# Kernel optimization log

Hardware: AMD Instinct MI355X
Metric: run time of the kernel (lower is better)

The kernel has to match this reference:

```python
import jax, jax.numpy as jnp
import numpy as np

B, S, D = 4, 4096, 2048
NUM_MODALITIES = 2


def setup_inputs() -> dict:
    key = jax.random.key(0)
    k_x, k_t, k_w0, k_b0, k_w1, k_b1 = jax.random.split(key, 6)
    scale = 1.0 / np.sqrt(D)
    return {
        "hidden_states": jax.random.normal(k_x, (B, S, D), dtype=jnp.float32),
        "type_ids": jax.random.randint(k_t, (B, S), 0, NUM_MODALITIES, dtype=jnp.int32),
        "W0": jax.random.uniform(k_w0, (D, D), jnp.float32, -scale, scale),
        "b0": jax.random.uniform(k_b0, (D,), jnp.float32, -scale, scale),
        "W1": jax.random.uniform(k_w1, (D, D), jnp.float32, -scale, scale),
        "b1": jax.random.uniform(k_b1, (D,), jnp.float32, -scale, scale),
    }


def reference(hidden_states, type_ids, W0, b0, W1, b1):
    # Original: gather tokens where type_ids == i, apply expert i's Linear,
    # scatter into a zero-init [B, S, out_dim] buffer. The masks partition
    # all tokens, so this equals a masked mixture of the two dense GEMMs.
    y0 = jnp.einsum("bsd,ed->bse", hidden_states, W0) + b0  # expert 0
    y1 = jnp.einsum("bsd,ed->bse", hidden_states, W1) + b1  # expert 1
    m0 = (type_ids == 0)[..., None]
    m1 = (type_ids == 1)[..., None]
    zero = jnp.zeros((), dtype=y0.dtype)
    return jnp.where(m0, y0, zero) + jnp.where(m1, y1, zero)
```

## Files before the change

kernel.cpp:

```cpp
#include <hip/hip_runtime.h>
#include <hip/hip_bf16.h>
#include <stdint.h>


#define T_TOK 16384
#define DDIM  2048
#define NT_K  32
#define NT_D  64
#define MT    64
#define NTILE 8

typedef __attribute__((ext_vector_type(4))) float          f32x4;
typedef __attribute__((ext_vector_type(8))) short          bf16x8;
typedef __attribute__((ext_vector_type(2))) unsigned int   u32x2;

#define WS_HBF   0ull
#define WS_W0BF  67108864ull
#define WS_W1BF  75497472ull
#define WS_META  83886080ull
#define WS_IDX   83886208ull
#define WS_NEED  (WS_IDX + 65536ull)

__device__ __forceinline__ unsigned short cvt1_bf16(float f) {
  unsigned u = __builtin_bit_cast(unsigned, f);
  unsigned rnd = 0x7fffu + ((u >> 16) & 1u);
  return (unsigned short)((u + rnd) >> 16);
}

__device__ __forceinline__ void gload_lds16(const void* g, void* l) {
  __builtin_amdgcn_global_load_lds(
      (const __attribute__((address_space(1))) unsigned int*)g,
      (__attribute__((address_space(3))) unsigned int*)l, 16, 0, 0);
}

#define BAR()     asm volatile("s_barrier" ::: "memory")
#define VMCNT2()  asm volatile("s_waitcnt vmcnt(2)" ::: "memory")
#define VMCNT4()  asm volatile("s_waitcnt vmcnt(4)" ::: "memory")
#define VMCNT6()  asm volatile("s_waitcnt vmcnt(6)" ::: "memory")
#define VMCNT0()  asm volatile("s_waitcnt vmcnt(0)" ::: "memory")
#define LGKM0()   asm volatile("s_waitcnt lgkmcnt(0)" ::: "memory")
#define SCHEDBAR() __builtin_amdgcn_sched_barrier(0)

__global__ void k_prep(const float* __restrict__ H, const float* __restrict__ W0,
                       const float* __restrict__ W1, const int* __restrict__ typ,
                       unsigned short* __restrict__ Hbf,
                       unsigned short* __restrict__ W0bf,
                       unsigned short* __restrict__ W1bf,
                       int* __restrict__ meta) {
  const int gid = blockIdx.x * blockDim.x + threadIdx.x;
  if (gid < T_TOK && typ[gid] == 0) atomicAdd(&meta[0], 1);
  const int nH = T_TOK * DDIM / 4;
  const int nW = DDIM * DDIM / 4;
  const int total = nH + 2 * nW;
  const int stride = gridDim.x * blockDim.x;
  for (int i = gid; i < total; i += stride) {
    const float* s; unsigned short* d; int j;
    if (i < nH)           { s = H;  d = Hbf;  j = i; }
    else if (i < nH + nW) { s = W0; d = W0bf; j = i - nH; }
    else                  { s = W1; d = W1bf; j = i - nH - nW; }
    f32x4 v = ((const f32x4*)s)[j];
    unsigned p0 = (unsigned)cvt1_bf16(v[0]) | ((unsigned)cvt1_bf16(v[1]) << 16);
    unsigned p1 = (unsigned)cvt1_bf16(v[2]) | ((unsigned)cvt1_bf16(v[3]) << 16);
    u32x2 o; o[0] = p0; o[1] = p1;
    ((u32x2*)d)[j] = o;
  }
}

__global__ void k_scatter(const int* __restrict__ typ, int* __restrict__ meta,
                          int* __restrict__ idx) {
  int i = blockIdx.x * blockDim.x + threadIdx.x;
  if (i >= T_TOK) return;
  int c0 = meta[0];
  int t = typ[i];
  int pos = (t == 0) ? atomicAdd(&meta[2], 1) : c0 + atomicAdd(&meta[3], 1);
  idx[pos] = i;
}

__global__ __launch_bounds__(512) void k_gemm256(
    const unsigned short* __restrict__ Hbf,
    const unsigned short* __restrict__ W0bf,
    const unsigned short* __restrict__ W1bf,
    const float* __restrict__ B0, const float* __restrict__ B1,
    const int* __restrict__ meta, const int* __restrict__ idx,
    float* __restrict__ OUT)
{
  __shared__ char lds[131072];

  const int orig = blockIdx.x;
  const int wg = (orig & 7) * 64 + (orig >> 3);
  int my = wg >> 3;
  const int bx = wg & 7;

  const int c0 = meta[0];
  int ms = c0 >> 8; if (ms > MT - 1) ms = MT - 1;
  my = (my == 0) ? ms : (my == ms) ? 0 : my;

  const int tid  = threadIdx.x;
  const int lane = tid & 63;
  const int wid  = tid >> 6;
  const int wr   = wid >> 2;
  const int wc   = wid & 3;
  const int fr   = lane & 15;
  const int g    = lane >> 4;

  const int start = my * 256;
  const int isDual = (start < c0 && c0 < start + 256) ? 1 : 0;
  const int e0    = (start >= c0) ? 1 : 0;
  const int colBase = bx * 256;

  const int cs = (lane & 3) ^ ((lane >> 3) & 3);
  const char* aS[2];
  int rt[2];
#pragma unroll
  for (int l = 0; l < 2; ++l) {
    int ch = 2 * wid + l;
    rt[l] = ch * 16 + (lane >> 2);
    int orow = idx[start + rt[l]];
    aS[l] = (const char*)Hbf + (size_t)orow * 4096 + cs * 16;
  }
  const int chB = (2 * wid) * 1024;

  const int sw = (g ^ ((fr >> 1) & 3)) << 4;
  int aF[8], bF[4];
#pragma unroll
  for (int m = 0; m < 8; ++m) aF[m] = ((wr * 128 + m * 16 + fr) << 6) + sw;
#pragma unroll
  for (int n = 0; n < 4; ++n) bF[n] = ((wc * 64 + n * 16 + fr) << 6) + sw;

  f32x4 acc[8][4];
#pragma unroll
  for (int m = 0; m < 8; ++m)
#pragma unroll
    for (int n = 0; n < 4; ++n) acc[m][n] = (f32x4)0.0f;

  int cols[4];
#pragma unroll
  for (int n = 0; n < 4; ++n) cols[n] = colBase + wc * 64 + n * 16 + fr;

  if (!isDual) {
    const unsigned short* Wb = e0 ? W1bf : W0bf;
    const char* wS[2];
#pragma unroll
    for (int l = 0; l < 2; ++l)
      wS[l] = (const char*)(Wb + (size_t)(colBase + rt[l]) * DDIM) + cs * 16;

    auto STAGE_A = [&](int d, int kh, int tn) {
      char* dst = lds + (d << 15) + (kh << 14) + chB;
      int ko = tn * 128 + kh * 64;
      gload_lds16(aS[0] + ko, dst);
      gload_lds16(aS[1] + ko, dst + 1024);
    };
    auto STAGE_B = [&](int d, int kh, int tn) {
      char* dst = lds + 65536 + (d << 15) + (kh << 14) + chB;
      int ko = tn * 128 + kh * 64;
      gload_lds16(wS[0] + ko, dst);
      gload_lds16(wS[1] + ko, dst + 1024);
    };

    STAGE_A(0, 0, 0); STAGE_B(0, 0, 0); STAGE_A(0, 1, 0); STAGE_B(0, 1, 0);
    VMCNT4();
    BAR();

#pragma unroll 2
    for (int t = 0; t < NT_K; ++t) {
      const int c = t & 1, d = c ^ 1;
      int t1 = t + 1; if (t1 == NT_K) t1 = NT_K - 1;
      const char* Ak0 = lds + (c << 15);
      const char* Ak1 = Ak0 + 16384;
      const char* Bk0 = lds + 65536 + (c << 15);
      const char* Bk1 = Bk0 + 16384;

      bf16x8 a[8], bb0, bb1;

#pragma unroll
      for (int m = 0; m < 8; ++m) a[m] = *(const bf16x8*)(Ak0 + aF[m]);
      bb0 = *(const bf16x8*)(Bk0 + bF[0]);
      bb1 = *(const bf16x8*)(Bk0 + bF[1]);
      STAGE_A(d, 0, t1);
      BAR(); LGKM0(); SCHEDBAR();
      __builtin_amdgcn_s_setprio(1);
#pragma unroll
      for (int m = 0; m < 8; ++m) {
        acc[m][0] = __builtin_amdgcn_mfma_f32_16x16x32_bf16(a[m], bb0, acc[m][0], 0, 0, 0);
        acc[m][1] = __builtin_amdgcn_mfma_f32_16x16x32_bf16(a[m], bb1, acc[m][1], 0, 0, 0);
      }
      __builtin_amdgcn_s_setprio(0);

      bb0 = *(const bf16x8*)(Bk0 + bF[2]);
      bb1 = *(const bf16x8*)(Bk0 + bF[3]);
      VMCNT2();
      STAGE_B(d, 0, t1);
      BAR(); LGKM0(); SCHEDBAR();
      __builtin_amdgcn_s_setprio(1);
#pragma unroll
      for (int m = 0; m < 8; ++m) {
        acc[m][2] = __builtin_amdgcn_mfma_f32_16x16x32_bf16(a[m], bb0, acc[m][2], 0, 0, 0);
        acc[m][3] = __builtin_amdgcn_mfma_f32_16x16x32_bf16(a[m], bb1, acc[m][3], 0, 0, 0);
      }
      __builtin_amdgcn_s_setprio(0);

#pragma unroll
      for (int m = 0; m < 8; ++m) a[m] = *(const bf16x8*)(Ak1 + aF[m]);
      bb0 = *(const bf16x8*)(Bk1 + bF[0]);
      bb1 = *(const bf16x8*)(Bk1 + bF[1]);
      STAGE_A(d, 1, t1);
      BAR(); LGKM0(); SCHEDBAR();
      __builtin_amdgcn_s_setprio(1);
#pragma unroll
      for (int m = 0; m < 8; ++m) {
        acc[m][0] = __builtin_amdgcn_mfma_f32_16x16x32_bf16(a[m], bb0, acc[m][0], 0, 0, 0);
        acc[m][1] = __builtin_amdgcn_mfma_f32_16x16x32_bf16(a[m], bb1, acc[m][1], 0, 0, 0);
      }
      __builtin_amdgcn_s_setprio(0);

      bb0 = *(const bf16x8*)(Bk1 + bF[2]);
      bb1 = *(const bf16x8*)(Bk1 + bF[3]);
      VMCNT2();
      STAGE_B(d, 1, t1);
      BAR(); LGKM0(); SCHEDBAR();
      __builtin_amdgcn_s_setprio(1);
#pragma unroll
      for (int m = 0; m < 8; ++m) {
        acc[m][2] = __builtin_amdgcn_mfma_f32_16x16x32_bf16(a[m], bb0, acc[m][2], 0, 0, 0);
        acc[m][3] = __builtin_amdgcn_mfma_f32_16x16x32_bf16(a[m], bb1, acc[m][3], 0, 0, 0);
      }
      __builtin_amdgcn_s_setprio(0);
    }

    VMCNT0();

    const float* Bv = e0 ? B1 : B0;
    float bias[4];
#pragma unroll
    for (int n = 0; n < 4; ++n) bias[n] = Bv[cols[n]];
#pragma unroll
    for (int m = 0; m < 8; ++m) {
      int lb = wr * 128 + m * 16 + (g << 2);
#pragma unroll
      for (int j = 0; j < 4; ++j) {
        int orow = idx[start + lb + j];
        float* op = OUT + (size_t)orow * DDIM;
#pragma unroll
        for (int n = 0; n < 4; ++n) op[cols[n]] = acc[m][n][j] + bias[n];
      }
    }
  } else {
    const char* wS0[2]; const char* wS1[2];
#pragma unroll
    for (int l = 0; l < 2; ++l) {
      wS0[l] = (const char*)(W0bf + (size_t)(colBase + rt[l]) * DDIM) + cs * 16;
      wS1[l] = (const char*)(W1bf + (size_t)(colBase + rt[l]) * DDIM) + cs * 16;
    }
    const int lo_w = c0 - start - wr * 128;
    int mmix = 8;
    if (lo_w > 0 && lo_w < 128 && (lo_w & 15)) mmix = lo_w >> 4;

    f32x4 accX[4];
#pragma unroll
    for (int n = 0; n < 4; ++n) accX[n] = (f32x4)0.0f;

    auto DSTAGE = [&](int d, int tn) {
      int ko = tn * 64;
      char* ad  = lds + (d << 14) + chB;
      char* b0d = lds + 32768 + (d << 14) + chB;
      char* b1d = lds + 65536 + (d << 14) + chB;
      gload_lds16(aS[0] + ko, ad);
      gload_lds16(aS[1] + ko, ad + 1024);
      gload_lds16(wS0[0] + ko, b0d);
      gload_lds16(wS0[1] + ko, b0d + 1024);
      gload_lds16(wS1[0] + ko, b1d);
      gload_lds16(wS1[1] + ko, b1d + 1024);
    };

    DSTAGE(0, 0);
    for (int t = 0; t < NT_D; ++t) {
      const int c = t & 1, d = c ^ 1;
      int t1 = t + 1; if (t1 == NT_D) t1 = NT_D - 1;
      DSTAGE(d, t1);
      VMCNT6();
      BAR();
      const char* Ac  = lds + (c << 14);
      const char* B0c = lds + 32768 + (c << 14);
      const char* B1c = lds + 65536 + (c << 14);
      bf16x8 a[8], b0f[4], b1f[4];
#pragma unroll
      for (int m = 0; m < 8; ++m) a[m] = *(const bf16x8*)(Ac + aF[m]);
#pragma unroll
      for (int n = 0; n < 4; ++n) {
        b0f[n] = *(const bf16x8*)(B0c + bF[n]);
        b1f[n] = *(const bf16x8*)(B1c + bF[n]);
      }
      LGKM0(); SCHEDBAR();
      __builtin_amdgcn_s_setprio(1);
#pragma unroll
      for (int m = 0; m < 8; ++m) {
        if (m == mmix) {
#pragma unroll
          for (int n = 0; n < 4; ++n) {
            acc[m][n] = __builtin_amdgcn_mfma_f32_16x16x32_bf16(a[m], b0f[n], acc[m][n], 0, 0, 0);
            accX[n]   = __builtin_amdgcn_mfma_f32_16x16x32_bf16(a[m], b1f[n], accX[n],   0, 0, 0);
          }
        } else if (m * 16 >= lo_w) {
#pragma unroll
          for (int n = 0; n < 4; ++n)
            acc[m][n] = __builtin_amdgcn_mfma_f32_16x16x32_bf16(a[m], b1f[n], acc[m][n], 0, 0, 0);
        } else {
#pragma unroll
          for (int n = 0; n < 4; ++n)
            acc[m][n] = __builtin_amdgcn_mfma_f32_16x16x32_bf16(a[m], b0f[n], acc[m][n], 0, 0, 0);
        }
      }
      __builtin_amdgcn_s_setprio(0);
      BAR();
    }
    VMCNT0();

    float bias0v[4], bias1v[4];
#pragma unroll
    for (int n = 0; n < 4; ++n) { bias0v[n] = B0[cols[n]]; bias1v[n] = B1[cols[n]]; }
#pragma unroll
    for (int m = 0; m < 8; ++m) {
      int lb = wr * 128 + m * 16 + (g << 2);
      if (m == mmix) {
#pragma unroll
        for (int j = 0; j < 4; ++j) {
          int p = start + lb + j;
          int orow = idx[p];
          float* op = OUT + (size_t)orow * DDIM;
          if (p >= c0) {
#pragma unroll
            for (int n = 0; n < 4; ++n) op[cols[n]] = accX[n][j] + bias1v[n];
          } else {
#pragma unroll
            for (int n = 0; n < 4; ++n) op[cols[n]] = acc[m][n][j] + bias0v[n];
          }
        }
      } else {
        int em = (m * 16 >= lo_w) ? 1 : 0;
#pragma unroll
        for (int j = 0; j < 4; ++j) {
          int orow = idx[start + lb + j];
          float* op = OUT + (size_t)orow * DDIM;
#pragma unroll
          for (int n = 0; n < 4; ++n)
            op[cols[n]] = acc[m][n][j] + (em ? bias1v[n] : bias0v[n]);
        }
      }
    }
  }
}

#define BMd 64
#define BNd 64
#define BKd 32
#define LDW 36

__device__ __forceinline__ bf16x8 cvt_bf16x8(f32x4 lo, f32x4 hi) {
  bf16x8 r;
#pragma unroll
  for (int i = 0; i < 4; ++i) {
    r[i]     = (short)cvt1_bf16(lo[i]);
    r[i + 4] = (short)cvt1_bf16(hi[i]);
  }
  return r;
}

__global__ __launch_bounds__(256, 2) void mot_mfma_diag(
    const float* __restrict__ H,  const int* __restrict__ TYP,
    const float* __restrict__ W0, const float* __restrict__ B0,
    const float* __restrict__ W1, const float* __restrict__ B1,
    float* __restrict__ OUT)
{
  __shared__ float As[BMd * LDW];
  __shared__ float W0s[BNd * LDW];
  __shared__ float W1s[BNd * LDW];

  const int tid = threadIdx.x;
  const int rowBase = blockIdx.y * BMd;
  const int colBase = blockIdx.x * BNd;
  const int srow  = tid >> 3;
  const int scol4 = (tid & 7) << 2;
  const float* hA  = H  + (size_t)(rowBase + srow) * DDIM + scol4;
  const float* hW0 = W0 + (size_t)(colBase + srow) * DDIM + scol4;
  const float* hW1 = W1 + (size_t)(colBase + srow) * DDIM + scol4;

  const int lane = tid & 63;
  const int w    = tid >> 6;
  const int fr   = lane & 15;
  const int g    = lane >> 4;

  f32x4 acc0[4], acc1[4];
#pragma unroll
  for (int m = 0; m < 4; ++m) { acc0[m] = (f32x4)0.0f; acc1[m] = (f32x4)0.0f; }

  for (int k0 = 0; k0 < DDIM; k0 += BKd) {
    f32x4 va[2], v0[2], v1[2];
#pragma unroll
    for (int p = 0; p < 2; ++p) {
      va[p] = *(const f32x4*)(hA  + (size_t)p * 32 * DDIM);
      v0[p] = *(const f32x4*)(hW0 + (size_t)p * 32 * DDIM);
      v1[p] = *(const f32x4*)(hW1 + (size_t)p * 32 * DDIM);
    }
    hA += BKd; hW0 += BKd; hW1 += BKd;
    __syncthreads();
#pragma unroll
    for (int p = 0; p < 2; ++p) {
      int r = srow + 32 * p;
      *(f32x4*)(&As [r * LDW + scol4]) = va[p];
      *(f32x4*)(&W0s[r * LDW + scol4]) = v0[p];
      *(f32x4*)(&W1s[r * LDW + scol4]) = v1[p];
    }
    __syncthreads();

    bf16x8 af[4];
#pragma unroll
    for (int m = 0; m < 4; ++m) {
      const float* ap = &As[(m * 16 + fr) * LDW + g * 8];
      af[m] = cvt_bf16x8(*(const f32x4*)ap, *(const f32x4*)(ap + 4));
    }
    const float* b0p = &W0s[(w * 16 + fr) * LDW + g * 8];
    const float* b1p = &W1s[(w * 16 + fr) * LDW + g * 8];
    bf16x8 bf0 = cvt_bf16x8(*(const f32x4*)b0p, *(const f32x4*)(b0p + 4));
    bf16x8 bf1 = cvt_bf16x8(*(const f32x4*)b1p, *(const f32x4*)(b1p + 4));
#pragma unroll
    for (int m = 0; m < 4; ++m) {
      acc0[m] = __builtin_amdgcn_mfma_f32_16x16x32_bf16(af[m], bf0, acc0[m], 0, 0, 0);
      acc1[m] = __builtin_amdgcn_mfma_f32_16x16x32_bf16(af[m], bf1, acc1[m], 0, 0, 0);
    }
  }

  const int col = colBase + w * 16 + fr;
  const float bz0 = B0[col];
  const float bz1 = B1[col];
#pragma unroll
  for (int m = 0; m < 4; ++m)
#pragma unroll
    for (int j = 0; j < 4; ++j) {
      int row = rowBase + m * 16 + (g << 2) + j;
      int t = TYP[row];
      OUT[(size_t)row * DDIM + col] = (t == 0) ? (acc0[m][j] + bz0) : (acc1[m][j] + bz1);
    }
}

extern "C" void kernel_launch(void* const* d_in, const int* in_sizes, int n_in,
                              void* d_out, int out_size, void* d_ws, size_t ws_size,
                              hipStream_t stream) {
  const float* H   = (const float*)d_in[0];
  const int*   TYP = (const int*)  d_in[1];
  const float* W0  = (const float*)d_in[2];
  const float* B0v = (const float*)d_in[3];
  const float* W1  = (const float*)d_in[4];
  const float* B1v = (const float*)d_in[5];
  float* OUT = (float*)d_out;

  if (ws_size < WS_NEED) {
    dim3 grid(DDIM / BNd, T_TOK / BMd);
    mot_mfma_diag<<<grid, dim3(256), 0, stream>>>(H, TYP, W0, B0v, W1, B1v, OUT);
    return;
  }

  unsigned short* Hbf  = (unsigned short*)((char*)d_ws + WS_HBF);
  unsigned short* W0bf = (unsigned short*)((char*)d_ws + WS_W0BF);
  unsigned short* W1bf = (unsigned short*)((char*)d_ws + WS_W1BF);
  int* meta = (int*)((char*)d_ws + WS_META);
  int* idx  = (int*)((char*)d_ws + WS_IDX);

  hipMemsetAsync(meta, 0, 16, stream);
  k_prep   <<<4096, 256, 0, stream>>>(H, W0, W1, TYP, Hbf, W0bf, W1bf, meta);
  k_scatter<<<64,   256, 0, stream>>>(TYP, meta, idx);
  k_gemm256<<<MT * NTILE, 512, 0, stream>>>(Hbf, W0bf, W1bf, B0v, B1v, meta, idx, OUT);
}
```

Measured before the change: 218.5 us.

## Fuse fp32-to-bf16 conversion of activations into GEMM A-tile staging

Removes the separate pass that converts hidden states to bf16 in a workspace. The GEMM now loads fp32 rows into registers, packs them with v_cvt_pk_bf16_f32, and writes them to LDS, prefetching two k-steps ahead. This drops a full read and write of the 128 MB activation tensor plus the re-read of the bf16 copy, and the prep kernel now converts only the weights. In exchange the GEMM reads twice as many A bytes, converts every A tile once per column block (8 times in total), and the pipeline's waitcnt and barrier placement is reworked, which could expose load latency.

New measurement: 221.2 us. About the same (+1.2%).

```diff
diff --git a/kernel.cpp b/kernel.cpp
--- a/kernel.cpp
+++ b/kernel.cpp
@@ -13,12 +13,12 @@
 typedef __attribute__((ext_vector_type(4))) float          f32x4;
 typedef __attribute__((ext_vector_type(8))) short          bf16x8;
 typedef __attribute__((ext_vector_type(2))) unsigned int   u32x2;
-
-#define WS_HBF   0ull
-#define WS_W0BF  67108864ull
-#define WS_W1BF  75497472ull
-#define WS_META  83886080ull
-#define WS_IDX   83886208ull
+typedef __attribute__((ext_vector_type(4))) unsigned int   u32x4;
+
+#define WS_W0BF  0ull
+#define WS_W1BF  8388608ull
+#define WS_META  16777216ull
+#define WS_IDX   16777344ull
 #define WS_NEED  (WS_IDX + 65536ull)
 
 __device__ __forceinline__ unsigned short cvt1_bf16(float f) {
@@ -27,6 +27,12 @@
   return (unsigned short)((u + rnd) >> 16);
 }
 
+__device__ __forceinline__ unsigned pk2(float lo, float hi) {
+  unsigned r;
+  asm("v_cvt_pk_bf16_f32 %0, %1, %2" : "=v"(r) : "v"(lo), "v"(hi));
+  return r;
+}
+
 __device__ __forceinline__ void gload_lds16(const void* g, void* l) {
   __builtin_amdgcn_global_load_lds(
       (const __attribute__((address_space(1))) unsigned int*)g,
@@ -34,30 +40,25 @@
 }
 
 #define BAR()     asm volatile("s_barrier" ::: "memory")
-#define VMCNT2()  asm volatile("s_waitcnt vmcnt(2)" ::: "memory")
 #define VMCNT4()  asm volatile("s_waitcnt vmcnt(4)" ::: "memory")
-#define VMCNT6()  asm volatile("s_waitcnt vmcnt(6)" ::: "memory")
+#define VMCNT8()  asm volatile("s_waitcnt vmcnt(8)" ::: "memory")
 #define VMCNT0()  asm volatile("s_waitcnt vmcnt(0)" ::: "memory")
 #define LGKM0()   asm volatile("s_waitcnt lgkmcnt(0)" ::: "memory")
 #define SCHEDBAR() __builtin_amdgcn_sched_barrier(0)
 
-__global__ void k_prep(const float* __restrict__ H, const float* __restrict__ W0,
-                       const float* __restrict__ W1, const int* __restrict__ typ,
-                       unsigned short* __restrict__ Hbf,
-                       unsigned short* __restrict__ W0bf,
-                       unsigned short* __restrict__ W1bf,
-                       int* __restrict__ meta) {
+__global__ void k_wprep(const float* __restrict__ W0, const float* __restrict__ W1,
+                        const int* __restrict__ typ,
+                        unsigned short* __restrict__ W0bf,
+                        unsigned short* __restrict__ W1bf,
+                        int* __restrict__ meta) {
   const int gid = blockIdx.x * blockDim.x + threadIdx.x;
   if (gid < T_TOK && typ[gid] == 0) atomicAdd(&meta[0], 1);
-  const int nH = T_TOK * DDIM / 4;
   const int nW = DDIM * DDIM / 4;
-  const int total = nH + 2 * nW;
   const int stride = gridDim.x * blockDim.x;
-  for (int i = gid; i < total; i += stride) {
-    const float* s; unsigned short* d; int j;
-    if (i < nH)           { s = H;  d = Hbf;  j = i; }
-    else if (i < nH + nW) { s = W0; d = W0bf; j = i - nH; }
-    else                  { s = W1; d = W1bf; j = i - nH - nW; }
+  for (int i = gid; i < 2 * nW; i += stride) {
+    const float* s = (i < nW) ? W0 : W1;
+    unsigned short* d = (i < nW) ? W0bf : W1bf;
+    int j = (i < nW) ? i : i - nW;
     f32x4 v = ((const f32x4*)s)[j];
     unsigned p0 = (unsigned)cvt1_bf16(v[0]) | ((unsigned)cvt1_bf16(v[1]) << 16);
     unsigned p1 = (unsigned)cvt1_bf16(v[2]) | ((unsigned)cvt1_bf16(v[3]) << 16);
@@ -77,7 +78,7 @@
 }
 
 __global__ __launch_bounds__(512) void k_gemm256(
-    const unsigned short* __restrict__ Hbf,
+    const float* __restrict__ H,
     const unsigned short* __restrict__ W0bf,
     const unsigned short* __restrict__ W1bf,
     const float* __restrict__ B0, const float* __restrict__ B1,
@@ -109,14 +110,14 @@
   const int colBase = bx * 256;
 
   const int cs = (lane & 3) ^ ((lane >> 3) & 3);
-  const char* aS[2];
+  const char* aS32[2];
   int rt[2];
 #pragma unroll
   for (int l = 0; l < 2; ++l) {
     int ch = 2 * wid + l;
     rt[l] = ch * 16 + (lane >> 2);
     int orow = idx[start + rt[l]];
-    aS[l] = (const char*)Hbf + (size_t)orow * 4096 + cs * 16;
+    aS32[l] = (const char*)H + (size_t)orow * 8192 + cs * 32;
   }
   const int chB = (2 * wid) * 1024;
 
@@ -144,11 +145,30 @@
     for (int l = 0; l < 2; ++l)
       wS[l] = (const char*)(Wb + (size_t)(colBase + rt[l]) * DDIM) + cs * 16;
 
-    auto STAGE_A = [&](int d, int kh, int tn) {
-      char* dst = lds + (d << 15) + (kh << 14) + chB;
-      int ko = tn * 128 + kh * 64;
-      gload_lds16(aS[0] + ko, dst);
-      gload_lds16(aS[1] + ko, dst + 1024);
+    f32x4 av[2][2][2];
+
+    auto ALOAD = [&](int tn) {
+#pragma unroll
+      for (int l = 0; l < 2; ++l)
+#pragma unroll
+        for (int kh = 0; kh < 2; ++kh) {
+          const char* p = aS32[l] + tn * 256 + kh * 128;
+          av[l][kh][0] = *(const f32x4*)p;
+          av[l][kh][1] = *(const f32x4*)(p + 16);
+        }
+    };
+    auto AWRITE = [&](int d) {
+#pragma unroll
+      for (int l = 0; l < 2; ++l)
+#pragma unroll
+        for (int kh = 0; kh < 2; ++kh) {
+          u32x4 w;
+          w[0] = pk2(av[l][kh][0][0], av[l][kh][0][1]);
+          w[1] = pk2(av[l][kh][0][2], av[l][kh][0][3]);
+          w[2] = pk2(av[l][kh][1][0], av[l][kh][1][1]);
+          w[3] = pk2(av[l][kh][1][2], av[l][kh][1][3]);
+          *(u32x4*)(lds + (d << 15) + (kh << 14) + (2 * wid + l) * 1024 + lane * 16) = w;
+        }
     };
     auto STAGE_B = [&](int d, int kh, int tn) {
       char* dst = lds + 65536 + (d << 15) + (kh << 14) + chB;
@@ -157,14 +177,20 @@
       gload_lds16(wS[1] + ko, dst + 1024);
     };
 
-    STAGE_A(0, 0, 0); STAGE_B(0, 0, 0); STAGE_A(0, 1, 0); STAGE_B(0, 1, 0);
-    VMCNT4();
+    ALOAD(0);
+    VMCNT0();
+    AWRITE(0);
+    STAGE_B(0, 0, 0); STAGE_B(0, 1, 0);
+    ALOAD(1);
+    VMCNT8();
+    LGKM0();
     BAR();
 
 #pragma unroll 2
     for (int t = 0; t < NT_K; ++t) {
       const int c = t & 1, d = c ^ 1;
       int t1 = t + 1; if (t1 == NT_K) t1 = NT_K - 1;
+      int t2 = t + 2; if (t2 >= NT_K) t2 = NT_K - 1;
       const char* Ak0 = lds + (c << 15);
       const char* Ak1 = Ak0 + 16384;
       const char* Bk0 = lds + 65536 + (c << 15);
@@ -176,7 +202,7 @@
       for (int m = 0; m < 8; ++m) a[m] = *(const bf16x8*)(Ak0 + aF[m]);
       bb0 = *(const bf16x8*)(Bk0 + bF[0]);
       bb1 = *(const bf16x8*)(Bk0 + bF[1]);
-      STAGE_A(d, 0, t1);
+      STAGE_B(d, 0, t1);
       BAR(); LGKM0(); SCHEDBAR();
       __builtin_amdgcn_s_setprio(1);
 #pragma unroll
@@ -188,8 +214,7 @@
 
       bb0 = *(const bf16x8*)(Bk0 + bF[2]);
       bb1 = *(const bf16x8*)(Bk0 + bF[3]);
-      VMCNT2();
-      STAGE_B(d, 0, t1);
+      STAGE_B(d, 1, t1);
       BAR(); LGKM0(); SCHEDBAR();
       __builtin_amdgcn_s_setprio(1);
 #pragma unroll
@@ -203,8 +228,10 @@
       for (int m = 0; m < 8; ++m) a[m] = *(const bf16x8*)(Ak1 + aF[m]);
       bb0 = *(const bf16x8*)(Bk1 + bF[0]);
       bb1 = *(const bf16x8*)(Bk1 + bF[1]);
-      STAGE_A(d, 1, t1);
-      BAR(); LGKM0(); SCHEDBAR();
+      VMCNT4();
+      AWRITE(d);
+      LGKM0(); SCHEDBAR();
+      BAR();
       __builtin_amdgcn_s_setprio(1);
 #pragma unroll
       for (int m = 0; m < 8; ++m) {
@@ -215,8 +242,8 @@
 
       bb0 = *(const bf16x8*)(Bk1 + bF[2]);
       bb1 = *(const bf16x8*)(Bk1 + bF[3]);
-      VMCNT2();
-      STAGE_B(d, 1, t1);
+      ALOAD(t2);
+      VMCNT8();
       BAR(); LGKM0(); SCHEDBAR();
       __builtin_amdgcn_s_setprio(1);
 #pragma unroll
@@ -259,26 +286,48 @@
 #pragma unroll
     for (int n = 0; n < 4; ++n) accX[n] = (f32x4)0.0f;
 
-    auto DSTAGE = [&](int d, int tn) {
-      int ko = tn * 64;
-      char* ad  = lds + (d << 14) + chB;
+    f32x4 avd[2][2];
+    auto ALOADD = [&](int tn) {
+#pragma unroll
+      for (int l = 0; l < 2; ++l) {
+        const char* p = aS32[l] + tn * 128;
+        avd[l][0] = *(const f32x4*)p;
+        avd[l][1] = *(const f32x4*)(p + 16);
+      }
+    };
+    auto AWRITED = [&](int d) {
+#pragma unroll
+      for (int l = 0; l < 2; ++l) {
+        u32x4 w;
+        w[0] = pk2(avd[l][0][0], avd[l][0][1]);
+        w[1] = pk2(avd[l][0][2], avd[l][0][3]);
+        w[2] = pk2(avd[l][1][0], avd[l][1][1]);
+        w[3] = pk2(avd[l][1][2], avd[l][1][3]);
+        *(u32x4*)(lds + (d << 14) + (2 * wid + l) * 1024 + lane * 16) = w;
+      }
+    };
+    auto STAGE_BD = [&](int d, int tn) {
       char* b0d = lds + 32768 + (d << 14) + chB;
       char* b1d = lds + 65536 + (d << 14) + chB;
-      gload_lds16(aS[0] + ko, ad);
-      gload_lds16(aS[1] + ko, ad + 1024);
-      gload_lds16(wS0[0] + ko, b0d);
-      gload_lds16(wS0[1] + ko, b0d + 1024);
-      gload_lds16(wS1[0] + ko, b1d);
-      gload_lds16(wS1[1] + ko, b1d + 1024);
+      gload_lds16(wS0[0] + tn * 64, b0d);
+      gload_lds16(wS0[1] + tn * 64, b0d + 1024);
+      gload_lds16(wS1[0] + tn * 64, b1d);
+      gload_lds16(wS1[1] + tn * 64, b1d + 1024);
     };
 
-    DSTAGE(0, 0);
+    ALOADD(0);
+    VMCNT0();
+    AWRITED(0);
+    STAGE_BD(0, 0);
+    ALOADD(1);
+    VMCNT4();
+    LGKM0();
+    BAR();
+
     for (int t = 0; t < NT_D; ++t) {
       const int c = t & 1, d = c ^ 1;
       int t1 = t + 1; if (t1 == NT_D) t1 = NT_D - 1;
-      DSTAGE(d, t1);
-      VMCNT6();
-      BAR();
+      int t2 = t + 2; if (t2 >= NT_D) t2 = NT_D - 1;
       const char* Ac  = lds + (c << 14);
       const char* B0c = lds + 32768 + (c << 14);
       const char* B1c = lds + 65536 + (c << 14);
@@ -290,6 +339,10 @@
         b0f[n] = *(const bf16x8*)(B0c + bF[n]);
         b1f[n] = *(const bf16x8*)(B1c + bF[n]);
       }
+      STAGE_BD(d, t1);
+      VMCNT4();
+      AWRITED(d);
+      ALOADD(t2);
       LGKM0(); SCHEDBAR();
       __builtin_amdgcn_s_setprio(1);
 #pragma unroll
@@ -311,6 +364,7 @@
         }
       }
       __builtin_amdgcn_s_setprio(0);
+      VMCNT4();
       BAR();
     }
     VMCNT0();
@@ -459,14 +513,13 @@
     return;
   }
 
-  unsigned short* Hbf  = (unsigned short*)((char*)d_ws + WS_HBF);
   unsigned short* W0bf = (unsigned short*)((char*)d_ws + WS_W0BF);
   unsigned short* W1bf = (unsigned short*)((char*)d_ws + WS_W1BF);
   int* meta = (int*)((char*)d_ws + WS_META);
   int* idx  = (int*)((char*)d_ws + WS_IDX);
 
   hipMemsetAsync(meta, 0, 16, stream);
-  k_prep   <<<4096, 256, 0, stream>>>(H, W0, W1, TYP, Hbf, W0bf, W1bf, meta);
+  k_wprep  <<<1024, 256, 0, stream>>>(W0, W1, TYP, W0bf, W1bf, meta);
   k_scatter<<<64,   256, 0, stream>>>(TYP, meta, idx);
-  k_gemm256<<<MT * NTILE, 512, 0, stream>>>(Hbf, W0bf, W1bf, B0v, B1v, meta, idx, OUT);
-}
+  k_gemm256<<<MT * NTILE, 512, 0, stream>>>(H, W0bf, W1bf, B0v, B1v, meta, idx, OUT);
+}
```

## Fuse token scatter into prep kernel and split GEMM k-step into two B halves

Applied to the files above, without the earlier changes.

The token-index scatter moves into the bf16 conversion kernel: type-0 tokens are filled from the front of the index array and type-1 tokens from the back, which removes one kernel launch and one dependent pass over type_ids. In the GEMM main loop, each k-step now loads B fragments in two halves of two columns each, with MFMAs in between. The next-stage global-to-LDS prefetch is issued after the current A/B LDS reads, and there is a full vmcnt(0) wait mid-iteration. This is meant to cut live vector registers and reorder load/compute overlap, but the prefetch now overlaps only the first half of the MFMAs.

After: 215.7 us. About the same (-1.3%).

```diff
diff --git a/kernel.cpp b/kernel.cpp
--- a/kernel.cpp
+++ b/kernel.cpp
@@ -36,7 +36,6 @@
 #define BAR()     asm volatile("s_barrier" ::: "memory")
 #define VMCNT2()  asm volatile("s_waitcnt vmcnt(2)" ::: "memory")
 #define VMCNT4()  asm volatile("s_waitcnt vmcnt(4)" ::: "memory")
-#define VMCNT6()  asm volatile("s_waitcnt vmcnt(6)" ::: "memory")
 #define VMCNT0()  asm volatile("s_waitcnt vmcnt(0)" ::: "memory")
 #define LGKM0()   asm volatile("s_waitcnt lgkmcnt(0)" ::: "memory")
 #define SCHEDBAR() __builtin_amdgcn_sched_barrier(0)
@@ -46,9 +45,14 @@
                        unsigned short* __restrict__ Hbf,
                        unsigned short* __restrict__ W0bf,
                        unsigned short* __restrict__ W1bf,
-                       int* __restrict__ meta) {
+                       int* __restrict__ meta, int* __restrict__ idx) {
   const int gid = blockIdx.x * blockDim.x + threadIdx.x;
-  if (gid < T_TOK && typ[gid] == 0) atomicAdd(&meta[0], 1);
+  if (gid < T_TOK) {
+    int t = typ[gid];
+    int pos = (t == 0) ? atomicAdd(&meta[0], 1)
+                       : (T_TOK - 1) - atomicAdd(&meta[1], 1);
+    idx[pos] = gid;
+  }
   const int nH = T_TOK * DDIM / 4;
   const int nW = DDIM * DDIM / 4;
   const int total = nH + 2 * nW;
@@ -66,16 +70,6 @@
   }
 }
 
-__global__ void k_scatter(const int* __restrict__ typ, int* __restrict__ meta,
-                          int* __restrict__ idx) {
-  int i = blockIdx.x * blockDim.x + threadIdx.x;
-  if (i >= T_TOK) return;
-  int c0 = meta[0];
-  int t = typ[i];
-  int pos = (t == 0) ? atomicAdd(&meta[2], 1) : c0 + atomicAdd(&meta[3], 1);
-  idx[pos] = i;
-}
-
 __global__ __launch_bounds__(512) void k_gemm256(
     const unsigned short* __restrict__ Hbf,
     const unsigned short* __restrict__ W0bf,
@@ -273,45 +267,66 @@
     };
 
     DSTAGE(0, 0);
+    VMCNT0();
+    BAR();
+
     for (int t = 0; t < NT_D; ++t) {
       const int c = t & 1, d = c ^ 1;
       int t1 = t + 1; if (t1 == NT_D) t1 = NT_D - 1;
-      DSTAGE(d, t1);
-      VMCNT6();
-      BAR();
       const char* Ac  = lds + (c << 14);
       const char* B0c = lds + 32768 + (c << 14);
       const char* B1c = lds + 65536 + (c << 14);
-      bf16x8 a[8], b0f[4], b1f[4];
+      bf16x8 a[8], b0a, b0b, b1a, b1b;
+
 #pragma unroll
       for (int m = 0; m < 8; ++m) a[m] = *(const bf16x8*)(Ac + aF[m]);
-#pragma unroll
-      for (int n = 0; n < 4; ++n) {
-        b0f[n] = *(const bf16x8*)(B0c + bF[n]);
-        b1f[n] = *(const bf16x8*)(B1c + bF[n]);
-      }
-      LGKM0(); SCHEDBAR();
+      b0a = *(const bf16x8*)(B0c + bF[0]);
+      b0b = *(const bf16x8*)(B0c + bF[1]);
+      b1a = *(const bf16x8*)(B1c + bF[0]);
+      b1b = *(const bf16x8*)(B1c + bF[1]);
+      DSTAGE(d, t1);
+      BAR(); LGKM0(); SCHEDBAR();
       __builtin_amdgcn_s_setprio(1);
 #pragma unroll
       for (int m = 0; m < 8; ++m) {
         if (m == mmix) {
-#pragma unroll
-          for (int n = 0; n < 4; ++n) {
-            acc[m][n] = __builtin_amdgcn_mfma_f32_16x16x32_bf16(a[m], b0f[n], acc[m][n], 0, 0, 0);
-            accX[n]   = __builtin_amdgcn_mfma_f32_16x16x32_bf16(a[m], b1f[n], accX[n],   0, 0, 0);
-          }
+          acc[m][0] = __builtin_amdgcn_mfma_f32_16x16x32_bf16(a[m], b0a, acc[m][0], 0, 0, 0);
+          acc[m][1] = __builtin_amdgcn_mfma_f32_16x16x32_bf16(a[m], b0b, acc[m][1], 0, 0, 0);
+          accX[0]   = __builtin_amdgcn_mfma_f32_16x16x32_bf16(a[m], b1a, accX[0],   0, 0, 0);
+          accX[1]   = __builtin_amdgcn_mfma_f32_16x16x32_bf16(a[m], b1b, accX[1],   0, 0, 0);
         } else if (m * 16 >= lo_w) {
-#pragma unroll
-          for (int n = 0; n < 4; ++n)
-            acc[m][n] = __builtin_amdgcn_mfma_f32_16x16x32_bf16(a[m], b1f[n], acc[m][n], 0, 0, 0);
+          acc[m][0] = __builtin_amdgcn_mfma_f32_16x16x32_bf16(a[m], b1a, acc[m][0], 0, 0, 0);
+          acc[m][1] = __builtin_amdgcn_mfma_f32_16x16x32_bf16(a[m], b1b, acc[m][1], 0, 0, 0);
         } else {
-#pragma unroll
-          for (int n = 0; n < 4; ++n)
-            acc[m][n] = __builtin_amdgcn_mfma_f32_16x16x32_bf16(a[m], b0f[n], acc[m][n], 0, 0, 0);
+          acc[m][0] = __builtin_amdgcn_mfma_f32_16x16x32_bf16(a[m], b0a, acc[m][0], 0, 0, 0);
+          acc[m][1] = __builtin_amdgcn_mfma_f32_16x16x32_bf16(a[m], b0b, acc[m][1], 0, 0, 0);
         }
       }
       __builtin_amdgcn_s_setprio(0);
-      BAR();
+
+      b0a = *(const bf16x8*)(B0c + bF[2]);
+      b0b = *(const bf16x8*)(B0c + bF[3]);
+      b1a = *(const bf16x8*)(B1c + bF[2]);
+      b1b = *(const bf16x8*)(B1c + bF[3]);
+      VMCNT0();
+      BAR(); LGKM0(); SCHEDBAR();
+      __builtin_amdgcn_s_setprio(1);
+#pragma unroll
+      for (int m = 0; m < 8; ++m) {
+        if (m == mmix) {
+          acc[m][2] = __builtin_amdgcn_mfma_f32_16x16x32_bf16(a[m], b0a, acc[m][2], 0, 0, 0);
+          acc[m][3] = __builtin_amdgcn_mfma_f32_16x16x32_bf16(a[m], b0b, acc[m][3], 0, 0, 0);
+          accX[2]   = __builtin_amdgcn_mfma_f32_16x16x32_bf16(a[m], b1a, accX[2],   0, 0, 0);
+          accX[3]   = __builtin_amdgcn_mfma_f32_16x16x32_bf16(a[m], b1b, accX[3],   0, 0, 0);
+        } else if (m * 16 >= lo_w) {
+          acc[m][2] = __builtin_amdgcn_mfma_f32_16x16x32_bf16(a[m], b1a, acc[m][2], 0, 0, 0);
+          acc[m][3] = __builtin_amdgcn_mfma_f32_16x16x32_bf16(a[m], b1b, acc[m][3], 0, 0, 0);
+        } else {
+          acc[m][2] = __builtin_amdgcn_mfma_f32_16x16x32_bf16(a[m], b0a, acc[m][2], 0, 0, 0);
+          acc[m][3] = __builtin_amdgcn_mfma_f32_16x16x32_bf16(a[m], b0b, acc[m][3], 0, 0, 0);
+        }
+      }
+      __builtin_amdgcn_s_setprio(0);
     }
     VMCNT0();
 
@@ -466,7 +481,6 @@
   int* idx  = (int*)((char*)d_ws + WS_IDX);
 
   hipMemsetAsync(meta, 0, 16, stream);
-  k_prep   <<<4096, 256, 0, stream>>>(H, W0, W1, TYP, Hbf, W0bf, W1bf, meta);
-  k_scatter<<<64,   256, 0, stream>>>(TYP, meta, idx);
+  k_prep<<<4096, 256, 0, stream>>>(H, W0, W1, TYP, Hbf, W0bf, W1bf, meta, idx);
   k_gemm256<<<MT * NTILE, 512, 0, stream>>>(Hbf, W0bf, W1bf, B0v, B1v, meta, idx, OUT);
 }
```

## Triple-buffer mixed-tile GEMM pipeline and fold token scatter into prep kernel

Applied to the files above, without the earlier changes.

The prep kernel now builds the token index list itself, placing type-0 tokens from the front and type-1 tokens from the back, so the separate scatter launch is gone. In the GEMM's mixed-tile path, LDS staging moves from double to triple buffering (LDS grows to 144KB), with the prefetch two steps ahead issued after the fragment reads. The goal is to hide global-load latency better and save a kernel launch. The cost is more LDS per block and a different order for type-1 indices, which the GEMM must still handle correctly.

After: 215.9 us. Within noise of the previous version (-1.2%).

```diff
diff --git a/kernel.cpp b/kernel.cpp
--- a/kernel.cpp
+++ b/kernel.cpp
@@ -46,9 +46,14 @@
                        unsigned short* __restrict__ Hbf,
                        unsigned short* __restrict__ W0bf,
                        unsigned short* __restrict__ W1bf,
-                       int* __restrict__ meta) {
+                       int* __restrict__ meta, int* __restrict__ idx) {
   const int gid = blockIdx.x * blockDim.x + threadIdx.x;
-  if (gid < T_TOK && typ[gid] == 0) atomicAdd(&meta[0], 1);
+  if (gid < T_TOK) {
+    int t = typ[gid];
+    int pos = (t == 0) ? atomicAdd(&meta[0], 1)
+                       : (T_TOK - 1) - atomicAdd(&meta[1], 1);
+    idx[pos] = gid;
+  }
   const int nH = T_TOK * DDIM / 4;
   const int nW = DDIM * DDIM / 4;
   const int total = nH + 2 * nW;
@@ -66,16 +71,6 @@
   }
 }
 
-__global__ void k_scatter(const int* __restrict__ typ, int* __restrict__ meta,
-                          int* __restrict__ idx) {
-  int i = blockIdx.x * blockDim.x + threadIdx.x;
-  if (i >= T_TOK) return;
-  int c0 = meta[0];
-  int t = typ[i];
-  int pos = (t == 0) ? atomicAdd(&meta[2], 1) : c0 + atomicAdd(&meta[3], 1);
-  idx[pos] = i;
-}
-
 __global__ __launch_bounds__(512) void k_gemm256(
     const unsigned short* __restrict__ Hbf,
     const unsigned short* __restrict__ W0bf,
@@ -84,7 +79,7 @@
     const int* __restrict__ meta, const int* __restrict__ idx,
     float* __restrict__ OUT)
 {
-  __shared__ char lds[131072];
+  __shared__ char lds[147456];
 
   const int orig = blockIdx.x;
   const int wg = (orig & 7) * 64 + (orig >> 3);
@@ -261,9 +256,9 @@
 
     auto DSTAGE = [&](int d, int tn) {
       int ko = tn * 64;
-      char* ad  = lds + (d << 14) + chB;
-      char* b0d = lds + 32768 + (d << 14) + chB;
-      char* b1d = lds + 65536 + (d << 14) + chB;
+      char* ad  = lds + d * 16384 + chB;
+      char* b0d = lds + 49152 + d * 16384 + chB;
+      char* b1d = lds + 98304 + d * 16384 + chB;
       gload_lds16(aS[0] + ko, ad);
       gload_lds16(aS[1] + ko, ad + 1024);
       gload_lds16(wS0[0] + ko, b0d);
@@ -272,16 +267,17 @@
       gload_lds16(wS1[1] + ko, b1d + 1024);
     };
 
-    DSTAGE(0, 0);
+    DSTAGE(0, 0); DSTAGE(1, 1);
+    VMCNT6();
+    BAR();
+
     for (int t = 0; t < NT_D; ++t) {
-      const int c = t & 1, d = c ^ 1;
-      int t1 = t + 1; if (t1 == NT_D) t1 = NT_D - 1;
-      DSTAGE(d, t1);
-      VMCNT6();
-      BAR();
-      const char* Ac  = lds + (c << 14);
-      const char* B0c = lds + 32768 + (c << 14);
-      const char* B1c = lds + 65536 + (c << 14);
+      const int c = t % 3;
+      const int d = (t + 2) % 3;
+      int t2 = t + 2; if (t2 >= NT_D) t2 = NT_D - 1;
+      const char* Ac  = lds + c * 16384;
+      const char* B0c = lds + 49152 + c * 16384;
+      const char* B1c = lds + 98304 + c * 16384;
       bf16x8 a[8], b0f[4], b1f[4];
 #pragma unroll
       for (int m = 0; m < 8; ++m) a[m] = *(const bf16x8*)(Ac + aF[m]);
@@ -290,7 +286,9 @@
         b0f[n] = *(const bf16x8*)(B0c + bF[n]);
         b1f[n] = *(const bf16x8*)(B1c + bF[n]);
       }
-      LGKM0(); SCHEDBAR();
+      DSTAGE(d, t2);
+      VMCNT6();
+      BAR(); LGKM0(); SCHEDBAR();
       __builtin_amdgcn_s_setprio(1);
 #pragma unroll
       for (int m = 0; m < 8; ++m) {
@@ -466,7 +464,6 @@
   int* idx  = (int*)((char*)d_ws + WS_IDX);
 
   hipMemsetAsync(meta, 0, 16, stream);
-  k_prep   <<<4096, 256, 0, stream>>>(H, W0, W1, TYP, Hbf, W0bf, W1bf, meta);
-  k_scatter<<<64,   256, 0, stream>>>(TYP, meta, idx);
+  k_prep<<<4096, 256, 0, stream>>>(H, W0, W1, TYP, Hbf, W0bf, W1bf, meta, idx);
   k_gemm256<<<MT * NTILE, 512, 0, stream>>>(Hbf, W0bf, W1bf, B0v, B1v, meta, idx, OUT);
 }
```
